# Performance work log

Measured on AMD Instinct MI355X. Metric: run time of the kernel, lower is better.

## Reference

```python
import jax, jax.numpy as jnp
import numpy as np

B, DIM = 8192, 64


def setup_inputs() -> dict:
    key = jax.random.key(0)
    m = jax.random.normal(key, (B, DIM, DIM), dtype=jnp.float32)
    # SPD input (covariance-like), positive trace so normA division is stable
    x = jnp.einsum('bij,bkj->bik', m, m) / DIM + 1e-3 * jnp.eye(DIM, dtype=jnp.float32)
    return {"x": x, "iterN": 5}


def reference(x, iterN):
    b, dim = x.shape[0], x.shape[1]
    I = jnp.eye(dim, dtype=x.dtype)  # [dim, dim]
    I3 = 3.0 * I                      # broadcast over batch
    # normA = (1/3) * sum(x * 3I) = trace(x)
    normA = jnp.trace(x, axis1=1, axis2=2)            # [B]
    A = x / normA[:, None, None]                       # [B, dim, dim]
    if iterN < 2:
        ZY = 0.5 * (I3 - A)
        YZY = jnp.matmul(A, ZY)
    else:
        ZY = 0.5 * (I3 - A)
        Y = jnp.matmul(A, ZY)
        Z = ZY
        for _ in range(1, iterN - 1):
            ZY = 0.5 * (I3 - jnp.matmul(Z, Y))
            Y = jnp.matmul(Y, ZY)
            Z = jnp.matmul(ZY, Z)
        YZY = 0.5 * jnp.matmul(Y, I3 - jnp.matmul(Z, Y))
    y = YZY * jnp.sqrt(normA)[:, None, None]
    return y
```

## Files before the change

### kernel.cpp

```cpp
#include <hip/hip_runtime.h>

#define DIM 64
#define LSTRIDE 68
#define PLANE (DIM * LSTRIDE)

typedef __attribute__((ext_vector_type(8))) short short8;
typedef __attribute__((ext_vector_type(16))) float f32x16;

#define MFMA(a, b, c) __builtin_amdgcn_mfma_f32_32x32x16_bf16((a), (b), (c), 0, 0, 0)

__device__ __forceinline__ unsigned int cvt_pk_bf16(float a, float b) {
    unsigned int r;
    asm("v_cvt_pk_bf16_f32 %0, %1, %2" : "=v"(r) : "v"(a), "v"(b));
    return r;
}

__device__ __forceinline__ void pack4(const float* v, uint2& hw, uint2& lw) {
    const unsigned int ph0 = cvt_pk_bf16(v[0], v[1]);
    const unsigned int ph1 = cvt_pk_bf16(v[2], v[3]);
    const float h0 = __uint_as_float(ph0 << 16);
    const float h1 = __uint_as_float(ph0 & 0xffff0000u);
    const float h2 = __uint_as_float(ph1 << 16);
    const float h3 = __uint_as_float(ph1 & 0xffff0000u);
    hw = make_uint2(ph0, ph1);
    lw = make_uint2(cvt_pk_bf16(v[0] - h0, v[1] - h1),
                    cvt_pk_bf16(v[2] - h2, v[3] - h3));
}

union FragU { short8 v; uint2 u2[2]; };

__device__ __forceinline__ short8 load_frag(const unsigned short* p) {
    FragU f;
    f.u2[0] = *(const uint2*)p;
    f.u2[1] = *(const uint2*)(p + 4);
    return f.v;
}

extern "C" __global__ void __launch_bounds__(256, 3)
isqrtm_kernel(const float* __restrict__ x, const int* __restrict__ iterN_p,
              float* __restrict__ out)
{
    __shared__ __align__(16) unsigned short pl[6][PLANE];

    const int t = threadIdx.x;
    const int b = blockIdx.x;
    const float* xg = x + (size_t)b * 4096;
    float* og = out + (size_t)b * 4096;
    const int iterN = iterN_p[0];

    const int lane = t & 63;

    float tv = xg[lane * 65];
    #pragma unroll
    for (int o = 32; o > 0; o >>= 1) tv += __shfl_down(tv, o);
    const float tr  = __shfl(tv, 0);
    const float inv = 1.0f / tr;
    const float sc  = sqrtf(tr);

    #pragma unroll
    for (int ch = 0; ch < 4; ++ch) {
        const int e  = ch * 1024 + t * 4;
        const int i  = e >> 6, j0 = e & 63;
        const float4 xv = *(const float4*)(xg + e);
        const float av[4] = { xv.x * inv, xv.y * inv, xv.z * inv, xv.w * inv };
        float zv[4];
        #pragma unroll
        for (int q = 0; q < 4; ++q)
            zv[q] = fmaf(-0.5f, av[q], (i == j0 + q) ? 1.5f : 0.0f);
        uint2 ahw, alw, zhw, zlw;
        pack4(av, ahw, alw);
        pack4(zv, zhw, zlw);
        const int ad = i * LSTRIDE + j0;
        *(uint2*)&pl[0][ad] = ahw;
        *(uint2*)&pl[1][ad] = alw;
        *(uint2*)&pl[4][ad] = zhw;
        *(uint2*)&pl[5][ad] = zlw;
    }
    __syncthreads();

    const int wv = t >> 6;
    const int wr = wv >> 1, wc = wv & 1;
    const int m  = lane & 31, hh = lane >> 5;
    const int ra = (32 * wr + m) * LSTRIDE + 8 * hh;
    const int rb = (32 * wc + m) * LSTRIDE + 8 * hh;
    const int dql = 32 * wc + m - 32 * wr - 4 * hh;

    short8 yh[4], yl[4];

    auto load_B = [&](int p_) {
        #pragma unroll
        for (int s = 0; s < 4; ++s) {
            yh[s] = load_frag(&pl[p_][rb + 16 * s]);
            yl[s] = load_frag(&pl[p_ + 1][rb + 16 * s]);
        }
    };

    auto matmul_cB = [&](int a_) -> f32x16 {
        f32x16 acc = {};
        #pragma unroll
        for (int s = 0; s < 4; ++s) {
            const short8 ah = load_frag(&pl[a_][ra + 16 * s]);
            const short8 al = load_frag(&pl[a_ + 1][ra + 16 * s]);
            acc = MFMA(ah, yh[s], acc);
            acc = MFMA(ah, yl[s], acc);
            acc = MFMA(al, yh[s], acc);
        }
        return acc;
    };

    auto matmul2_cB = [&](int b2_, f32x16& o1, f32x16& o2) {
        o1 = {}; o2 = {};
        #pragma unroll
        for (int s = 0; s < 4; ++s) {
            const short8 ah  = load_frag(&pl[0][ra + 16 * s]);
            const short8 al  = load_frag(&pl[1][ra + 16 * s]);
            const short8 b2h = load_frag(&pl[b2_][rb + 16 * s]);
            const short8 b2l = load_frag(&pl[b2_ + 1][rb + 16 * s]);
            o1 = MFMA(ah, yh[s], o1); o1 = MFMA(ah, yl[s], o1); o1 = MFMA(al, yh[s], o1);
            o2 = MFMA(ah, b2h, o2);   o2 = MFMA(ah, b2l, o2);   o2 = MFMA(al, b2h, o2);
        }
    };

    auto write_tile = [&](int p_, const f32x16& acc, bool zyform) {
        #pragma unroll
        for (int g = 0; g < 4; ++g) {
            float v[4];
            #pragma unroll
            for (int q = 0; q < 4; ++q) {
                v[q] = acc[4 * g + q];
                if (zyform)
                    v[q] = fmaf(-0.5f, v[q], (q + 8 * g == dql) ? 1.5f : 0.0f);
            }
            uint2 hw, lw;
            pack4(v, hw, lw);
            const int ad = (32 * wc + m) * LSTRIDE + (32 * wr + 8 * g + 4 * hh);
            *(uint2*)&pl[p_][ad]     = hw;
            *(uint2*)&pl[p_ + 1][ad] = lw;
        }
    };

    auto write_global = [&](const f32x16& acc, float scale) {
        #pragma unroll
        for (int g = 0; g < 4; ++g)
            #pragma unroll
            for (int q = 0; q < 4; ++q) {
                const int rl = q + 8 * g + 4 * hh;
                og[(32 * wr + rl) * 64 + 32 * wc + m] = acc[4 * g + q] * scale;
            }
    };

    {
        load_B(4);
        const f32x16 accY = matmul_cB(0);
        if (iterN < 2) { write_global(accY, sc); return; }
        write_tile(2, accY, false);
    }
    __syncthreads();

    for (int it = 1; it < iterN - 1; ++it) {
        load_B(2);
        const f32x16 T = matmul_cB(4);
        write_tile(0, T, true);
        __syncthreads();
        f32x16 nY, nZ;
        matmul2_cB(4, nY, nZ);
        __syncthreads();
        write_tile(2, nY, false);
        write_tile(4, nZ, false);
        __syncthreads();
    }

    {
        load_B(2);
        const f32x16 T = matmul_cB(4);
        write_tile(0, T, true);
        __syncthreads();
        const f32x16 O = matmul_cB(0);
        write_global(O, sc);
    }
}

extern "C" void kernel_launch(void* const* d_in, const int* in_sizes, int n_in,
                              void* d_out, int out_size, void* d_ws, size_t ws_size,
                              hipStream_t stream) {
    const float* x = (const float*)d_in[0];
    const int* iterN = (const int*)d_in[1];
    float* out = (float*)d_out;
    const int B = in_sizes[0] / (DIM * DIM);
    isqrtm_kernel<<<dim3(B), dim3(256), 0, stream>>>(x, iterN, out);
}
```

Measured before the change: 311.5 us.

## Exploit matrix symmetry to compute only three of four tiles with 192 threads

Because every iterate (Y, Z, ZY) of the Newton-Schulz iteration stays symmetric for SPD input, the kernel now computes only the upper-triangular 32x32 tiles (0,0), (0,1) and (1,1) using three waves instead of four. The off-diagonal wave also writes the transposed copy of its tile into shared memory and to the output. This removes a quarter of the MFMA work per block. The cost is scattered 16-bit transposed LDS stores, a change in launch bounds and occupancy, and reliance on symmetry holding within bf16-split rounding.

```diff
diff --git a/kernel.cpp b/kernel.cpp
--- a/kernel.cpp
+++ b/kernel.cpp
@@ -36,7 +36,7 @@
     return f.v;
 }
 
-extern "C" __global__ void __launch_bounds__(256, 3)
+extern "C" __global__ void __launch_bounds__(192, 2)
 isqrtm_kernel(const float* __restrict__ x, const int* __restrict__ iterN_p,
               float* __restrict__ out)
 {
@@ -57,9 +57,7 @@
     const float inv = 1.0f / tr;
     const float sc  = sqrtf(tr);
 
-    #pragma unroll
-    for (int ch = 0; ch < 4; ++ch) {
-        const int e  = ch * 1024 + t * 4;
+    auto build = [&](int e) {
         const int i  = e >> 6, j0 = e & 63;
         const float4 xv = *(const float4*)(xg + e);
         const float av[4] = { xv.x * inv, xv.y * inv, xv.z * inv, xv.w * inv };
@@ -75,11 +73,15 @@
         *(uint2*)&pl[1][ad] = alw;
         *(uint2*)&pl[4][ad] = zhw;
         *(uint2*)&pl[5][ad] = zlw;
-    }
+    };
+    #pragma unroll
+    for (int ch = 0; ch < 5; ++ch) build(ch * 768 + t * 4);
+    if (t < 64) build(3840 + t * 4);
     __syncthreads();
 
     const int wv = t >> 6;
-    const int wr = wv >> 1, wc = wv & 1;
+    const int wr = wv >> 1;
+    const int wc = (wv + 1) >> 1;
     const int m  = lane & 31, hh = lane >> 5;
     const int ra = (32 * wr + m) * LSTRIDE + 8 * hh;
     const int rb = (32 * wc + m) * LSTRIDE + 8 * hh;
@@ -136,17 +138,38 @@
             const int ad = (32 * wc + m) * LSTRIDE + (32 * wr + 8 * g + 4 * hh);
             *(uint2*)&pl[p_][ad]     = hw;
             *(uint2*)&pl[p_ + 1][ad] = lw;
+            if (wv == 1) {
+                const int ad2 = (8 * g + 4 * hh) * LSTRIDE + 32 + m;
+                unsigned short* ph = &pl[p_][ad2];
+                unsigned short* po = &pl[p_ + 1][ad2];
+                ph[0]           = (unsigned short)hw.x;
+                ph[LSTRIDE]     = (unsigned short)(hw.x >> 16);
+                ph[2 * LSTRIDE] = (unsigned short)hw.y;
+                ph[3 * LSTRIDE] = (unsigned short)(hw.y >> 16);
+                po[0]           = (unsigned short)lw.x;
+                po[LSTRIDE]     = (unsigned short)(lw.x >> 16);
+                po[2 * LSTRIDE] = (unsigned short)lw.y;
+                po[3 * LSTRIDE] = (unsigned short)(lw.y >> 16);
+            }
         }
     };
 
     auto write_global = [&](const f32x16& acc, float scale) {
         #pragma unroll
-        for (int g = 0; g < 4; ++g)
+        for (int g = 0; g < 4; ++g) {
             #pragma unroll
             for (int q = 0; q < 4; ++q) {
                 const int rl = q + 8 * g + 4 * hh;
                 og[(32 * wr + rl) * 64 + 32 * wc + m] = acc[4 * g + q] * scale;
             }
+            if (wv == 1) {
+                const float4 o4 = make_float4(acc[4 * g]     * scale,
+                                              acc[4 * g + 1] * scale,
+                                              acc[4 * g + 2] * scale,
+                                              acc[4 * g + 3] * scale);
+                *(float4*)&og[(32 + m) * 64 + 8 * g + 4 * hh] = o4;
+            }
+        }
     };
 
     {
@@ -187,5 +210,5 @@
     const int* iterN = (const int*)d_in[1];
     float* out = (float*)d_out;
     const int B = in_sizes[0] / (DIM * DIM);
-    isqrtm_kernel<<<dim3(B), dim3(256), 0, stream>>>(x, iterN, out);
-}
+    isqrtm_kernel<<<dim3(B), dim3(192), 0, stream>>>(x, iterN, out);
+}
```

After: 303.5 us. 2.6% less time.

## Keep each 64x64 matrix in one wavefront's registers, dropping LDS and block barriers

Applied to the files above, without the earlier changes.

Moves from one matrix per 256-thread block, with tiles shared through LDS, to one matrix per wavefront held entirely in registers as bf16 hi/lo MFMA fragments. Accumulator outputs are turned back into operand fragments with v_permlane32_swap, so most LDS round-trips and all __syncthreads are gone. A small per-wave LDS staging buffer is kept only for the Y update. This raises register pressure a lot (launch bounds drop to 2), and it assumes B is divisible by 4.

```diff
diff --git a/kernel.cpp b/kernel.cpp
--- a/kernel.cpp
+++ b/kernel.cpp
@@ -1,8 +1,4 @@
 #include <hip/hip_runtime.h>
-
-#define DIM 64
-#define LSTRIDE 68
-#define PLANE (DIM * LSTRIDE)
 
 typedef __attribute__((ext_vector_type(8))) short short8;
 typedef __attribute__((ext_vector_type(16))) float f32x16;
@@ -15,169 +11,201 @@
     return r;
 }
 
-__device__ __forceinline__ void pack4(const float* v, uint2& hw, uint2& lw) {
-    const unsigned int ph0 = cvt_pk_bf16(v[0], v[1]);
-    const unsigned int ph1 = cvt_pk_bf16(v[2], v[3]);
-    const float h0 = __uint_as_float(ph0 << 16);
-    const float h1 = __uint_as_float(ph0 & 0xffff0000u);
-    const float h2 = __uint_as_float(ph1 << 16);
-    const float h3 = __uint_as_float(ph1 & 0xffff0000u);
-    hw = make_uint2(ph0, ph1);
-    lw = make_uint2(cvt_pk_bf16(v[0] - h0, v[1] - h1),
-                    cvt_pk_bf16(v[2] - h2, v[3] - h3));
-}
-
-union FragU { short8 v; uint2 u2[2]; };
-
-__device__ __forceinline__ short8 load_frag(const unsigned short* p) {
-    FragU f;
-    f.u2[0] = *(const uint2*)p;
-    f.u2[1] = *(const uint2*)(p + 4);
-    return f.v;
-}
-
-extern "C" __global__ void __launch_bounds__(256, 3)
+#define SWAP_HALVES(a, b) asm("v_permlane32_swap_b32 %0, %1" : "+v"(a), "+v"(b))
+
+union FR { short8 v; unsigned int d[4]; };
+union U4 { short8 v; uint4 u; };
+
+struct Mat { short8 h[4][2]; short8 l[4][2]; };
+
+extern "C" __global__ void __launch_bounds__(256, 2)
 isqrtm_kernel(const float* __restrict__ x, const int* __restrict__ iterN_p,
               float* __restrict__ out)
 {
-    __shared__ __align__(16) unsigned short pl[6][PLANE];
+    __shared__ uint4 stg[4][4][4][64];
 
     const int t = threadIdx.x;
-    const int b = blockIdx.x;
-    const float* xg = x + (size_t)b * 4096;
-    float* og = out + (size_t)b * 4096;
+    const int wv = t >> 6, lane = t & 63;
+    const int m = lane & 31, h = lane >> 5;
+
     const int iterN = iterN_p[0];
-
-    const int lane = t & 63;
+    const size_t mat = (size_t)blockIdx.x * 4 + wv;
+    const float* xg = x + mat * 4096;
+    float* og = out + mat * 4096;
 
     float tv = xg[lane * 65];
     #pragma unroll
-    for (int o = 32; o > 0; o >>= 1) tv += __shfl_down(tv, o);
+    for (int off = 32; off > 0; off >>= 1) tv += __shfl_down(tv, off);
     const float tr  = __shfl(tv, 0);
     const float inv = 1.0f / tr;
     const float sc  = sqrtf(tr);
 
-    #pragma unroll
-    for (int ch = 0; ch < 4; ++ch) {
-        const int e  = ch * 1024 + t * 4;
-        const int i  = e >> 6, j0 = e & 63;
-        const float4 xv = *(const float4*)(xg + e);
-        const float av[4] = { xv.x * inv, xv.y * inv, xv.z * inv, xv.w * inv };
-        float zv[4];
-        #pragma unroll
-        for (int q = 0; q < 4; ++q)
-            zv[q] = fmaf(-0.5f, av[q], (i == j0 + q) ? 1.5f : 0.0f);
-        uint2 ahw, alw, zhw, zlw;
-        pack4(av, ahw, alw);
-        pack4(zv, zhw, zlw);
-        const int ad = i * LSTRIDE + j0;
-        *(uint2*)&pl[0][ad] = ahw;
-        *(uint2*)&pl[1][ad] = alw;
-        *(uint2*)&pl[4][ad] = zhw;
-        *(uint2*)&pl[5][ad] = zlw;
+    Mat Wm, Ym, Zm;
+
+    #pragma unroll
+    for (int I = 0; I < 2; ++I)
+    #pragma unroll
+    for (int J = 0; J < 2; ++J)
+    #pragma unroll
+    for (int s = 0; s < 2; ++s) {
+        const float* bp = xg + (32 * I + m) * 64 + 32 * J + 16 * s + 8 * h;
+        const float4 u0 = *(const float4*)bp;
+        const float4 u1 = *(const float4*)(bp + 4);
+        const float av[8] = { u0.x * inv, u0.y * inv, u0.z * inv, u0.w * inv,
+                              u1.x * inv, u1.y * inv, u1.z * inv, u1.w * inv };
+        float zv[8];
+        #pragma unroll
+        for (int i = 0; i < 8; ++i)
+            zv[i] = fmaf(-0.5f, av[i], (I == J && m == 16 * s + 8 * h + i) ? 1.5f : 0.0f);
+        FR ah, al, zh, zl;
+        #pragma unroll
+        for (int p = 0; p < 4; ++p) {
+            ah.d[p] = cvt_pk_bf16(av[2*p], av[2*p+1]);
+            al.d[p] = cvt_pk_bf16(av[2*p]   - __uint_as_float(ah.d[p] << 16),
+                                  av[2*p+1] - __uint_as_float(ah.d[p] & 0xffff0000u));
+            zh.d[p] = cvt_pk_bf16(zv[2*p], zv[2*p+1]);
+            zl.d[p] = cvt_pk_bf16(zv[2*p]   - __uint_as_float(zh.d[p] << 16),
+                                  zv[2*p+1] - __uint_as_float(zh.d[p] & 0xffff0000u));
+        }
+        Wm.h[2*I+J][s] = ah.v;  Wm.l[2*I+J][s] = al.v;
+        Zm.h[2*I+J][s] = zh.v;  Zm.l[2*I+J][s] = zl.v;
     }
-    __syncthreads();
-
-    const int wv = t >> 6;
-    const int wr = wv >> 1, wc = wv & 1;
-    const int m  = lane & 31, hh = lane >> 5;
-    const int ra = (32 * wr + m) * LSTRIDE + 8 * hh;
-    const int rb = (32 * wc + m) * LSTRIDE + 8 * hh;
-    const int dql = 32 * wc + m - 32 * wr - 4 * hh;
-
-    short8 yh[4], yl[4];
-
-    auto load_B = [&](int p_) {
-        #pragma unroll
-        for (int s = 0; s < 4; ++s) {
-            yh[s] = load_frag(&pl[p_][rb + 16 * s]);
-            yl[s] = load_frag(&pl[p_ + 1][rb + 16 * s]);
-        }
-    };
-
-    auto matmul_cB = [&](int a_) -> f32x16 {
-        f32x16 acc = {};
-        #pragma unroll
-        for (int s = 0; s < 4; ++s) {
-            const short8 ah = load_frag(&pl[a_][ra + 16 * s]);
-            const short8 al = load_frag(&pl[a_ + 1][ra + 16 * s]);
-            acc = MFMA(ah, yh[s], acc);
-            acc = MFMA(ah, yl[s], acc);
-            acc = MFMA(al, yh[s], acc);
-        }
-        return acc;
-    };
-
-    auto matmul2_cB = [&](int b2_, f32x16& o1, f32x16& o2) {
-        o1 = {}; o2 = {};
-        #pragma unroll
-        for (int s = 0; s < 4; ++s) {
-            const short8 ah  = load_frag(&pl[0][ra + 16 * s]);
-            const short8 al  = load_frag(&pl[1][ra + 16 * s]);
-            const short8 b2h = load_frag(&pl[b2_][rb + 16 * s]);
-            const short8 b2l = load_frag(&pl[b2_ + 1][rb + 16 * s]);
-            o1 = MFMA(ah, yh[s], o1); o1 = MFMA(ah, yl[s], o1); o1 = MFMA(al, yh[s], o1);
-            o2 = MFMA(ah, b2h, o2);   o2 = MFMA(ah, b2l, o2);   o2 = MFMA(al, b2h, o2);
-        }
-    };
-
-    auto write_tile = [&](int p_, const f32x16& acc, bool zyform) {
+
+    auto mmblk = [&](const Mat& L, const Mat& R, int I, int J) -> f32x16 {
+        f32x16 a = {};
+        #pragma unroll
+        for (int K = 0; K < 2; ++K)
+        #pragma unroll
+        for (int s = 0; s < 2; ++s) {
+            const short8 lh = L.h[2*I+K][s], ll = L.l[2*I+K][s];
+            const short8 rh = R.h[2*J+K][s], rl = R.l[2*J+K][s];
+            a = MFMA(lh, rh, a);
+            a = MFMA(lh, rl, a);
+            a = MFMA(ll, rh, a);
+        }
+        return a;
+    };
+
+    auto conv4 = [&](const f32x16& acc, int I, int J, bool wfold,
+                     short8& hs0, short8& hs1, short8& ls0, short8& ls1) {
+        unsigned int D01[4], D23[4], L01[4], L23[4];
         #pragma unroll
         for (int g = 0; g < 4; ++g) {
-            float v[4];
-            #pragma unroll
-            for (int q = 0; q < 4; ++q) {
-                v[q] = acc[4 * g + q];
-                if (zyform)
-                    v[q] = fmaf(-0.5f, v[q], (q + 8 * g == dql) ? 1.5f : 0.0f);
+            float v0 = acc[4*g+0], v1 = acc[4*g+1], v2 = acc[4*g+2], v3 = acc[4*g+3];
+            if (wfold) {
+                v0 = fmaf(-0.5f, v0, (I == J && 8*g + 4*h + 0 == m) ? 1.5f : 0.0f);
+                v1 = fmaf(-0.5f, v1, (I == J && 8*g + 4*h + 1 == m) ? 1.5f : 0.0f);
+                v2 = fmaf(-0.5f, v2, (I == J && 8*g + 4*h + 2 == m) ? 1.5f : 0.0f);
+                v3 = fmaf(-0.5f, v3, (I == J && 8*g + 4*h + 3 == m) ? 1.5f : 0.0f);
             }
-            uint2 hw, lw;
-            pack4(v, hw, lw);
-            const int ad = (32 * wc + m) * LSTRIDE + (32 * wr + 8 * g + 4 * hh);
-            *(uint2*)&pl[p_][ad]     = hw;
-            *(uint2*)&pl[p_ + 1][ad] = lw;
-        }
-    };
-
-    auto write_global = [&](const f32x16& acc, float scale) {
-        #pragma unroll
-        for (int g = 0; g < 4; ++g)
-            #pragma unroll
-            for (int q = 0; q < 4; ++q) {
-                const int rl = q + 8 * g + 4 * hh;
-                og[(32 * wr + rl) * 64 + 32 * wc + m] = acc[4 * g + q] * scale;
-            }
-    };
-
-    {
-        load_B(4);
-        const f32x16 accY = matmul_cB(0);
-        if (iterN < 2) { write_global(accY, sc); return; }
-        write_tile(2, accY, false);
+            D01[g] = cvt_pk_bf16(v0, v1);
+            D23[g] = cvt_pk_bf16(v2, v3);
+            L01[g] = cvt_pk_bf16(v0 - __uint_as_float(D01[g] << 16),
+                                 v1 - __uint_as_float(D01[g] & 0xffff0000u));
+            L23[g] = cvt_pk_bf16(v2 - __uint_as_float(D23[g] << 16),
+                                 v3 - __uint_as_float(D23[g] & 0xffff0000u));
+        }
+        SWAP_HALVES(D01[0], D01[1]); SWAP_HALVES(D23[0], D23[1]);
+        SWAP_HALVES(D01[2], D01[3]); SWAP_HALVES(D23[2], D23[3]);
+        SWAP_HALVES(L01[0], L01[1]); SWAP_HALVES(L23[0], L23[1]);
+        SWAP_HALVES(L01[2], L01[3]); SWAP_HALVES(L23[2], L23[3]);
+        FR f;
+        f.d[0]=D01[0]; f.d[1]=D23[0]; f.d[2]=D01[1]; f.d[3]=D23[1]; hs0 = f.v;
+        f.d[0]=D01[2]; f.d[1]=D23[2]; f.d[2]=D01[3]; f.d[3]=D23[3]; hs1 = f.v;
+        f.d[0]=L01[0]; f.d[1]=L23[0]; f.d[2]=L01[1]; f.d[3]=L23[1]; ls0 = f.v;
+        f.d[0]=L01[2]; f.d[1]=L23[2]; f.d[2]=L01[3]; f.d[3]=L23[3]; ls1 = f.v;
+    };
+
+    auto conv_store = [&](const f32x16& acc, Mat& D, int I, int J, bool wfold) {
+        short8 a, b, c, d;
+        conv4(acc, I, J, wfold, a, b, c, d);
+        D.h[2*J+I][0] = a; D.h[2*J+I][1] = b;
+        D.l[2*J+I][0] = c; D.l[2*J+I][1] = d;
+    };
+
+    auto conv_stage = [&](const f32x16& acc, int I, int J) {
+        short8 a, b, c, d;
+        conv4(acc, I, J, false, a, b, c, d);
+        U4 u;
+        u.v = a; stg[wv][2*J+I][0][lane] = u.u;
+        u.v = b; stg[wv][2*J+I][1][lane] = u.u;
+        u.v = c; stg[wv][2*J+I][2][lane] = u.u;
+        u.v = d; stg[wv][2*J+I][3][lane] = u.u;
+    };
+
+    auto out_block = [&](const f32x16& acc, int I, int J) {
+        float o[16];
+        #pragma unroll
+        for (int s = 0; s < 2; ++s)
+        #pragma unroll
+        for (int q = 0; q < 4; ++q) {
+            float a = acc[8*s + q] * sc;
+            float b = acc[8*s + 4 + q] * sc;
+            SWAP_HALVES(a, b);
+            o[8*s + q] = a;
+            o[8*s + 4 + q] = b;
+        }
+        float* ob = og + (32 * J + m) * 64 + 32 * I;
+        #pragma unroll
+        for (int s = 0; s < 2; ++s) {
+            *(float4*)(ob + 16*s + 8*h)     = make_float4(o[8*s+0], o[8*s+1], o[8*s+2], o[8*s+3]);
+            *(float4*)(ob + 16*s + 8*h + 4) = make_float4(o[8*s+4], o[8*s+5], o[8*s+6], o[8*s+7]);
+        }
+    };
+
+    if (iterN < 2) {
+        #pragma unroll
+        for (int I = 0; I < 2; ++I)
+        #pragma unroll
+        for (int J = 0; J < 2; ++J)
+            out_block(mmblk(Wm, Zm, I, J), I, J);
+        return;
     }
-    __syncthreads();
+    #pragma unroll
+    for (int I = 0; I < 2; ++I)
+    #pragma unroll
+    for (int J = 0; J < 2; ++J)
+        conv_store(mmblk(Wm, Zm, I, J), Ym, I, J, false);
 
     for (int it = 1; it < iterN - 1; ++it) {
-        load_B(2);
-        const f32x16 T = matmul_cB(4);
-        write_tile(0, T, true);
-        __syncthreads();
-        f32x16 nY, nZ;
-        matmul2_cB(4, nY, nZ);
-        __syncthreads();
-        write_tile(2, nY, false);
-        write_tile(4, nZ, false);
-        __syncthreads();
+        #pragma unroll
+        for (int I = 0; I < 2; ++I)
+        #pragma unroll
+        for (int J = 0; J < 2; ++J)
+            conv_store(mmblk(Zm, Ym, I, J), Wm, I, J, true);
+        #pragma unroll
+        for (int I = 0; I < 2; ++I)
+        #pragma unroll
+        for (int J = 0; J < 2; ++J)
+            conv_stage(mmblk(Ym, Wm, I, J), I, J);
+        f32x16 z00 = mmblk(Wm, Zm, 0, 0);
+        f32x16 z01 = mmblk(Wm, Zm, 0, 1);
+        f32x16 z10 = mmblk(Wm, Zm, 1, 0);
+        f32x16 z11 = mmblk(Wm, Zm, 1, 1);
+        conv_store(z00, Zm, 0, 0, false);
+        conv_store(z01, Zm, 0, 1, false);
+        conv_store(z10, Zm, 1, 0, false);
+        conv_store(z11, Zm, 1, 1, false);
+        #pragma unroll
+        for (int blk = 0; blk < 4; ++blk) {
+            U4 u;
+            u.u = stg[wv][blk][0][lane]; Ym.h[blk][0] = u.v;
+            u.u = stg[wv][blk][1][lane]; Ym.h[blk][1] = u.v;
+            u.u = stg[wv][blk][2][lane]; Ym.l[blk][0] = u.v;
+            u.u = stg[wv][blk][3][lane]; Ym.l[blk][1] = u.v;
+        }
     }
 
-    {
-        load_B(2);
-        const f32x16 T = matmul_cB(4);
-        write_tile(0, T, true);
-        __syncthreads();
-        const f32x16 O = matmul_cB(0);
-        write_global(O, sc);
-    }
+    #pragma unroll
+    for (int I = 0; I < 2; ++I)
+    #pragma unroll
+    for (int J = 0; J < 2; ++J)
+        conv_store(mmblk(Zm, Ym, I, J), Wm, I, J, true);
+    #pragma unroll
+    for (int I = 0; I < 2; ++I)
+    #pragma unroll
+    for (int J = 0; J < 2; ++J)
+        out_block(mmblk(Ym, Wm, I, J), I, J);
 }
 
 extern "C" void kernel_launch(void* const* d_in, const int* in_sizes, int n_in,
@@ -186,6 +214,6 @@
     const float* x = (const float*)d_in[0];
     const int* iterN = (const int*)d_in[1];
     float* out = (float*)d_out;
-    const int B = in_sizes[0] / (DIM * DIM);
-    isqrtm_kernel<<<dim3(B), dim3(256), 0, stream>>>(x, iterN, out);
+    const int B = in_sizes[0] / (64 * 64);
+    isqrtm_kernel<<<dim3(B / 4), dim3(256), 0, stream>>>(x, iterN, out);
 }
```

Result: slower. 396.4 us (+27.2%).
